# Kernel tuning notes

Hardware: AMD Instinct MI355X
Metric: run time of the kernel (lower is better)

Reference implementation:

```python
import jax, jax.numpy as jnp
import numpy as np

EPS = 1e-6  # LayerNorm eps, added to std as in annotated-transformer LayerNorm


def _layernorm(x, gamma, beta):
    # torch-style: a_2*(x-mean)/(std+eps)+b_2, std is UNBIASED (ddof=1)
    mu = x.mean(axis=-1, keepdims=True)
    std = jnp.sqrt(x.var(axis=-1, ddof=1, keepdims=True))
    return gamma * (x - mu) / (std + EPS) + beta


def setup_inputs() -> dict:
    key = jax.random.key(0)
    ks = jax.random.split(key, 6)
    B, S, E, V = 32, 2048, 512, 32000
    return {
        "hidden_state": jax.random.normal(ks[0], (B, 1, E), jnp.float32),
        "output_sequence": jax.random.randint(ks[1], (B, S), 0, V),
        "emb_out": jax.random.normal(ks[2], (V, E), jnp.float32) * 0.02,
        "W_dec": jax.random.normal(ks[3], (E, E), jnp.float32) / np.sqrt(E),
        "b_dec": jnp.zeros((E,), jnp.float32),
        "gamma": jnp.ones((E,), jnp.float32),
        "beta": jnp.zeros((E,), jnp.float32),
        "W_voc": jax.random.normal(ks[4], (E, V), jnp.float32) / np.sqrt(E),
        "b_voc": jnp.zeros((V,), jnp.float32),
    }


def reference(hidden_state, output_sequence, emb_out, W_dec, b_dec, gamma, beta, W_voc, b_voc):
    E = emb_out.shape[1]
    # Embeddings: lookup scaled by sqrt(embed_dim)
    x = emb_out[output_sequence] * jnp.sqrt(jnp.asarray(E, emb_out.dtype))  # [B,S,E]

    def step(z, xt):  # z: [B,E], xt: [B,E]
        z = z + xt
        z = z + z @ W_dec + b_dec  # decoder_transfer with residual
        z = _layernorm(z, gamma, beta)
        return z, None

    z0 = jnp.zeros((x.shape[0], E), x.dtype)
    z, _ = jax.lax.scan(step, z0, jnp.swapaxes(x, 0, 1))  # scan over S
    z = z[:, None, :]  # [B,1,E]
    # VocabLogits: linear + log_softmax
    y = jax.nn.log_softmax(z @ W_voc + b_voc, axis=-1)  # [B,1,V]
    return z, y
```

## Files before the change

### kernel.cpp

```cpp
#include <hip/hip_runtime.h>
#include <math.h>

typedef float v4 __attribute__((ext_vector_type(4)));
typedef unsigned long long u64;

static constexpr int B_ = 32;
static constexpr int S_ = 2048;
static constexpr int E_ = 512;
static constexpr int V_ = 32000;
static constexpr float EPS_ = 1e-6f;
static constexpr int NH_ = 8;
static constexpr int CH_ = 64;

__global__ __launch_bounds__(1024) void scan2b(
    const int* __restrict__ seq,
    const float* __restrict__ emb,
    const float* __restrict__ Wdec,
    const float* __restrict__ bdec,
    const float* __restrict__ gamma,
    const float* __restrict__ beta,
    float* __restrict__ zout,
    u64* __restrict__ zpub)
{
    __shared__ __align__(16) float zs[E_];
    __shared__ __align__(16) float part[NH_][CH_];
    __shared__ __align__(16) float zmbuf[E_];
    __shared__ int   seq_l[S_];

    const int bid  = blockIdx.x;
    const int b    = bid & 31;
    const int h    = bid >> 5;
    const int c0   = h * CH_;
    const int tid  = threadIdx.x;
    const int wv   = tid >> 6;
    const int lane = tid & 63;
    const int cg   = lane & 15;
    const int sub  = lane >> 4;
    const bool comp = (wv < 8);
    const int row0 = wv * 64 + sub * 16;

    v4 w[16];
    if (comp) {
        const float* wp = Wdec + (size_t)row0 * E_ + c0 + 4 * cg;
        #pragma unroll
        for (int q = 0; q < 16; ++q) {
            const float* p = wp + (size_t)q * E_;
            asm volatile("global_load_dwordx4 %0, %1, off\n\ts_waitcnt vmcnt(0)"
                         : "=v"(w[q]) : "v"(p));
        }
    }

    const int* seqb = seq + (size_t)b * S_;
    for (int i = tid; i < S_; i += 1024) seq_l[i] = seqb[i];

    const float gmm = (tid < E_) ? gamma[tid] : 0.f;
    const float btt = (tid < E_) ? beta[tid] : 0.f;
    const float bdr = (tid < CH_) ? bdec[c0 + tid] : 0.f;
    const float sqrtE = sqrtf(512.0f);
    u64* zpb = zpub + (size_t)b * 2 * E_;

    int fs = 0;
    if (wv >= 8 && wv < 15) { const int j = wv - 8; fs = j + ((j >= h) ? 1 : 0); }

    __syncthreads();
    if (tid < E_) zs[tid] = emb[(size_t)seq_l[0] * E_ + tid] * sqrtE;
    __syncthreads();

    for (int t = 0; t < S_; ++t) {
        const int p = t & 1;
        const unsigned tag = (unsigned)(t + 1);

        float e = 0.f;
        if (comp) {
            const int tn = seq_l[(t + 1 < S_) ? t + 1 : t];
            e = emb[(size_t)tn * E_ + tid];

            const v4 za = *(const v4*)&zs[row0];
            const v4 zb = *(const v4*)&zs[row0 + 4];
            const v4 zc = *(const v4*)&zs[row0 + 8];
            const v4 zd = *(const v4*)&zs[row0 + 12];
            v4 acc = za.x * w[0];
            acc += za.y * w[1];
            acc += za.z * w[2];
            acc += za.w * w[3];
            acc += zb.x * w[4];
            acc += zb.y * w[5];
            acc += zb.z * w[6];
            acc += zb.w * w[7];
            acc += zc.x * w[8];
            acc += zc.y * w[9];
            acc += zc.z * w[10];
            acc += zc.w * w[11];
            acc += zd.x * w[12];
            acc += zd.y * w[13];
            acc += zd.z * w[14];
            acc += zd.w * w[15];
            acc.x += __shfl_down(acc.x, 16);
            acc.y += __shfl_down(acc.y, 16);
            acc.z += __shfl_down(acc.z, 16);
            acc.w += __shfl_down(acc.w, 16);
            acc.x += __shfl_down(acc.x, 32);
            acc.y += __shfl_down(acc.y, 32);
            acc.z += __shfl_down(acc.z, 32);
            acc.w += __shfl_down(acc.w, 32);
            if (lane < 16) *(v4*)&part[wv][4 * cg] = acc;
        }
        __syncthreads();

        if (tid < CH_) {
            const float sum = ((part[0][tid] + part[1][tid])
                             + (part[2][tid] + part[3][tid]))
                            + ((part[4][tid] + part[5][tid])
                             + (part[6][tid] + part[7][tid]));
            const float zmid = zs[c0 + tid] + sum + bdr;
            union { float f; unsigned u; } cv; cv.f = zmid;
            __hip_atomic_store(&zpb[p * E_ + c0 + tid],
                               ((u64)tag << 32) | cv.u,
                               __ATOMIC_RELAXED, __HIP_MEMORY_SCOPE_AGENT);
            zmbuf[c0 + tid] = zmid;
        } else if (wv >= 8 && wv < 15) {
            const u64* ap = &zpb[p * E_ + fs * CH_ + lane];
            u64 s0 = __hip_atomic_load(ap, __ATOMIC_RELAXED,
                                       __HIP_MEMORY_SCOPE_AGENT);
            u64 s1 = __hip_atomic_load(ap, __ATOMIC_RELAXED,
                                       __HIP_MEMORY_SCOPE_AGENT);
            float val = 0.f;
            bool done = false;
            for (;;) {
                if (!done && (unsigned)(s0 >> 32) == tag) {
                    val = __uint_as_float((unsigned)s0); done = true;
                }
                if (__all(done)) break;
                s0 = __hip_atomic_load(ap, __ATOMIC_RELAXED,
                                       __HIP_MEMORY_SCOPE_AGENT);
                if (!done && (unsigned)(s1 >> 32) == tag) {
                    val = __uint_as_float((unsigned)s1); done = true;
                }
                if (__all(done)) break;
                s1 = __hip_atomic_load(ap, __ATOMIC_RELAXED,
                                       __HIP_MEMORY_SCOPE_AGENT);
            }
            zmbuf[fs * CH_ + lane] = val;
        }
        __syncthreads();

        if (comp) {
            float s = 0.f, q2 = 0.f;
            #pragma unroll
            for (int k = 0; k < 8; ++k) {
                const float v = zmbuf[lane + 64 * k];
                s += v; q2 += v * v;
            }
            #pragma unroll
            for (int m = 1; m < 64; m <<= 1) {
                s  += __shfl_xor(s, m);
                q2 += __shfl_xor(q2, m);
            }
            const float mu   = s * (1.0f / E_);
            const float var  = (q2 - s * mu) * (1.0f / (E_ - 1));
            const float invd = 1.0f / (sqrtf(var) + EPS_);
            const float zl   = gmm * (zmbuf[tid] - mu) * invd + btt;
            if (t == S_ - 1) {
                if (h == 0) zout[(size_t)b * E_ + tid] = zl;
            } else {
                zs[tid] = fmaf(e, sqrtE, zl);
            }
        }
    }
}

__global__ __launch_bounds__(512) void logits_k(
    const float* __restrict__ zfin,
    const float* __restrict__ Wvoc,
    const float* __restrict__ bvoc,
    float* __restrict__ y)
{
    const int tid = threadIdx.x;
    const int col = blockIdx.x * 128 + (tid & 127);
    const int bg  = (tid >> 7) * 8;

    float acc[8] = {0.f, 0.f, 0.f, 0.f, 0.f, 0.f, 0.f, 0.f};
    const float* wp = Wvoc + col;
    const float* zp = zfin + (size_t)bg * E_;

    for (int k = 0; k < E_; k += 4) {
        const float w0 = wp[(size_t)(k + 0) * V_];
        const float w1 = wp[(size_t)(k + 1) * V_];
        const float w2 = wp[(size_t)(k + 2) * V_];
        const float w3 = wp[(size_t)(k + 3) * V_];
        #pragma unroll
        for (int g = 0; g < 8; ++g) {
            acc[g] = fmaf(zp[g * E_ + k + 0], w0, acc[g]);
            acc[g] = fmaf(zp[g * E_ + k + 1], w1, acc[g]);
            acc[g] = fmaf(zp[g * E_ + k + 2], w2, acc[g]);
            acc[g] = fmaf(zp[g * E_ + k + 3], w3, acc[g]);
        }
    }
    const float bv = bvoc[col];
    #pragma unroll
    for (int g = 0; g < 8; ++g)
        y[(size_t)(bg + g) * V_ + col] = acc[g] + bv;
}

__global__ __launch_bounds__(1024) void lse_k(
    const float* __restrict__ y, float* __restrict__ corr)
{
    __shared__ float redm[16], redl[16];
    const int b = blockIdx.x;
    const int tid = threadIdx.x;
    const float* row = y + (size_t)b * V_;

    float m = -3.0e38f, l = 0.f;
    for (int v = tid; v < V_; v += 1024) {
        const float x = row[v];
        const float nm = fmaxf(m, x);
        l = l * __expf(m - nm) + __expf(x - nm);
        m = nm;
    }
    #pragma unroll
    for (int off = 32; off > 0; off >>= 1) {
        const float om = __shfl_down(m, off);
        const float ol = __shfl_down(l, off);
        const float nm = fmaxf(m, om);
        l = l * __expf(m - nm) + ol * __expf(om - nm);
        m = nm;
    }
    const int lane = tid & 63, wvv = tid >> 6;
    if (lane == 0) { redm[wvv] = m; redl[wvv] = l; }
    __syncthreads();
    if (tid == 0) {
        float M = redm[0], L = redl[0];
        for (int k = 1; k < 16; ++k) {
            const float nm = fmaxf(M, redm[k]);
            L = L * __expf(M - nm) + redl[k] * __expf(redm[k] - nm);
            M = nm;
        }
        corr[b] = M + logf(L);
    }
}

__global__ __launch_bounds__(256) void fix_k(
    float* __restrict__ y, const float* __restrict__ corr)
{
    const int idx = blockIdx.x * 256 + threadIdx.x;
    const size_t o = (size_t)idx * 4;
    const int b = (int)(o / V_);
    const float cr = corr[b];
    v4 v = *(v4*)(y + o);
    v = v - cr;
    *(v4*)(y + o) = v;
}

extern "C" void kernel_launch(void* const* d_in, const int* in_sizes, int n_in,
                              void* d_out, int out_size, void* d_ws, size_t ws_size,
                              hipStream_t stream)
{
    (void)in_sizes; (void)n_in; (void)out_size; (void)ws_size;
    const int*   seq  = (const int*)  d_in[1];
    const float* emb  = (const float*)d_in[2];
    const float* Wdec = (const float*)d_in[3];
    const float* bdec = (const float*)d_in[4];
    const float* gam  = (const float*)d_in[5];
    const float* bet  = (const float*)d_in[6];
    const float* Wvoc = (const float*)d_in[7];
    const float* bvoc = (const float*)d_in[8];

    float* out  = (float*)d_out;
    float* zout = out;
    float* y    = out + B_ * E_;

    const size_t exch_u64 = (size_t)B_ * 2 * E_;
    u64*   zpub = (u64*)d_ws;
    float* corr = (float*)((char*)d_ws + exch_u64 * sizeof(u64));

    hipMemsetAsync(zpub, 0, exch_u64 * sizeof(u64), stream);

    hipLaunchKernelGGL(scan2b, dim3(B_ * NH_), dim3(1024), 0, stream,
                       seq, emb, Wdec, bdec, gam, bet, zout, zpub);
    hipLaunchKernelGGL(logits_k, dim3(V_ / 128), dim3(512), 0, stream,
                       zout, Wvoc, bvoc, y);
    hipLaunchKernelGGL(lse_k, dim3(B_), dim3(1024), 0, stream, y, corr);
    hipLaunchKernelGGL(fix_k, dim3(1000), dim3(256), 0, stream, y, corr);
}
```

Baseline: 4.138 ms.

## Fold LayerNorm into decoder matvec and replace block barriers with flag-based sync

The scan kernel is restructured so the LayerNorm of the previous step is folded algebraically into the next matvec: W gets the identity added for the residual, the matvec runs on gamma-scaled unnormalized z, and mean and inverse std are applied afterwards as inv*(M - mu*G) plus the separately computed embedding matvec. Per-step __syncthreads are replaced by LDS flag handshakes between waves. Per-slice partial sums and sums of squares are published through global memory, so a dedicated wave can compute the statistics without a full-vector reduction. This aims to shorten the serial critical path of each recurrence step, at the cost of doing two matvecs per step, a more fragile spin-wait protocol, and different floating-point rounding.

```diff
diff --git a/kernel.cpp b/kernel.cpp
--- a/kernel.cpp
+++ b/kernel.cpp
@@ -12,7 +12,30 @@
 static constexpr int NH_ = 8;
 static constexpr int CH_ = 64;
 
-__global__ __launch_bounds__(1024) void scan2b(
+#define WG_ __HIP_MEMORY_SCOPE_WORKGROUP
+#define AG_ __HIP_MEMORY_SCOPE_AGENT
+
+static __device__ __forceinline__ v4 mv16(const v4* w, const float* zp) {
+    const v4 a = *(const v4*)(zp);
+    const v4 b = *(const v4*)(zp + 4);
+    const v4 c = *(const v4*)(zp + 8);
+    const v4 d = *(const v4*)(zp + 12);
+    v4 acc = a.x * w[0];
+    acc += a.y * w[1];  acc += a.z * w[2];  acc += a.w * w[3];
+    acc += b.x * w[4];  acc += b.y * w[5];  acc += b.z * w[6];  acc += b.w * w[7];
+    acc += c.x * w[8];  acc += c.y * w[9];  acc += c.z * w[10]; acc += c.w * w[11];
+    acc += d.x * w[12]; acc += d.y * w[13]; acc += d.z * w[14]; acc += d.w * w[15];
+    return acc;
+}
+static __device__ __forceinline__ v4 red2(v4 acc) {
+    acc.x += __shfl_down(acc.x, 16); acc.y += __shfl_down(acc.y, 16);
+    acc.z += __shfl_down(acc.z, 16); acc.w += __shfl_down(acc.w, 16);
+    acc.x += __shfl_down(acc.x, 32); acc.y += __shfl_down(acc.y, 32);
+    acc.z += __shfl_down(acc.z, 32); acc.w += __shfl_down(acc.w, 32);
+    return acc;
+}
+
+__global__ __launch_bounds__(1024) void scanfx(
     const int* __restrict__ seq,
     const float* __restrict__ emb,
     const float* __restrict__ Wdec,
@@ -22,10 +45,17 @@
     float* __restrict__ zout,
     u64* __restrict__ zpub)
 {
-    __shared__ __align__(16) float zs[E_];
+    __shared__ __align__(16) float zmG[2][E_];
+    __shared__ __align__(16) float xbuf[2][E_];
     __shared__ __align__(16) float part[NH_][CH_];
-    __shared__ __align__(16) float zmbuf[E_];
-    __shared__ int   seq_l[S_];
+    __shared__ __align__(16) float xpart[NH_][CH_];
+    __shared__ float munv[2][2];
+    __shared__ unsigned vrdy[2][NH_];
+    __shared__ unsigned rdone[NH_];
+    __shared__ unsigned mtag[2];
+    __shared__ unsigned hseen;
+    __shared__ unsigned cnt;
+    __shared__ int seq_l[S_];
 
     const int bid  = blockIdx.x;
     const int b    = bid & 31;
@@ -48,82 +78,127 @@
             asm volatile("global_load_dwordx4 %0, %1, off\n\ts_waitcnt vmcnt(0)"
                          : "=v"(w[q]) : "v"(p));
         }
+        const int cb = c0 + 4 * cg;
+        #pragma unroll
+        for (int q = 0; q < 16; ++q) {
+            const int r = row0 + q;
+            w[q].x += (r == cb + 0) ? 1.f : 0.f;
+            w[q].y += (r == cb + 1) ? 1.f : 0.f;
+            w[q].z += (r == cb + 2) ? 1.f : 0.f;
+            w[q].w += (r == cb + 3) ? 1.f : 0.f;
+        }
     }
 
     const int* seqb = seq + (size_t)b * S_;
     for (int i = tid; i < S_; i += 1024) seq_l[i] = seqb[i];
 
-    const float gmm = (tid < E_) ? gamma[tid] : 0.f;
-    const float btt = (tid < E_) ? beta[tid] : 0.f;
-    const float bdr = (tid < CH_) ? bdec[c0 + tid] : 0.f;
     const float sqrtE = sqrtf(512.0f);
+    const float gmm = comp ? gamma[tid] : 0.f;
+    const float btt = comp ? beta[tid]  : 0.f;
+    const float bd  = (wv == h) ? bdec[c0 + lane]  : 0.f;
+    const float gh  = (wv == h) ? gamma[c0 + lane] : 0.f;
+
+    int fs = 0; float gf = 0.f;
+    if (wv >= 8 && wv < 15) {
+        const int j = wv - 8; fs = j + ((j >= h) ? 1 : 0);
+        gf = gamma[fs * CH_ + lane];
+    }
+
     u64* zpb = zpub + (size_t)b * 2 * E_;
-
-    int fs = 0;
-    if (wv >= 8 && wv < 15) { const int j = wv - 8; fs = j + ((j >= h) ? 1 : 0); }
-
+    u64* zst = zpub + (size_t)B_ * 2 * E_ + (size_t)b * 32;
+
+    if (comp) { zmG[1][tid] = gamma[tid]; zmG[0][tid] = 0.f; }
+    if (tid < NH_) { vrdy[0][tid] = 0u; vrdy[1][tid] = 0u; rdone[tid] = 0u; }
+    if (tid == 0) {
+        mtag[0] = 0u; mtag[1] = 0u;
+        munv[1][0] = 0.f; munv[1][1] = 0.f;
+        munv[0][0] = 0.f; munv[0][1] = 0.f;
+        hseen = 0u; cnt = 0u;
+    }
     __syncthreads();
-    if (tid < E_) zs[tid] = emb[(size_t)seq_l[0] * E_ + tid] * sqrtE;
+    if (comp) xbuf[0][tid] = emb[(size_t)seq_l[0] * E_ + tid] * sqrtE;
+
+    float Gc = 0.f;
+    if (comp) {
+        v4 g = red2(mv16(w, &zmG[1][row0]));
+        if (lane < 16) *(v4*)&part[wv][4 * cg] = g;
+    }
     __syncthreads();
+    if (wv == h) {
+        Gc = ((part[0][lane] + part[1][lane]) + (part[2][lane] + part[3][lane]))
+           + ((part[4][lane] + part[5][lane]) + (part[6][lane] + part[7][lane]));
+    }
+    __syncthreads();
 
     for (int t = 0; t < S_; ++t) {
-        const int p = t & 1;
+        const int pt = t & 1, pp = pt ^ 1;
         const unsigned tag = (unsigned)(t + 1);
 
-        float e = 0.f;
         if (comp) {
-            const int tn = seq_l[(t + 1 < S_) ? t + 1 : t];
-            e = emb[(size_t)tn * E_ + tid];
-
-            const v4 za = *(const v4*)&zs[row0];
-            const v4 zb = *(const v4*)&zs[row0 + 4];
-            const v4 zc = *(const v4*)&zs[row0 + 8];
-            const v4 zd = *(const v4*)&zs[row0 + 12];
-            v4 acc = za.x * w[0];
-            acc += za.y * w[1];
-            acc += za.z * w[2];
-            acc += za.w * w[3];
-            acc += zb.x * w[4];
-            acc += zb.y * w[5];
-            acc += zb.z * w[6];
-            acc += zb.w * w[7];
-            acc += zc.x * w[8];
-            acc += zc.y * w[9];
-            acc += zc.z * w[10];
-            acc += zc.w * w[11];
-            acc += zd.x * w[12];
-            acc += zd.y * w[13];
-            acc += zd.z * w[14];
-            acc += zd.w * w[15];
-            acc.x += __shfl_down(acc.x, 16);
-            acc.y += __shfl_down(acc.y, 16);
-            acc.z += __shfl_down(acc.z, 16);
-            acc.w += __shfl_down(acc.w, 16);
-            acc.x += __shfl_down(acc.x, 32);
-            acc.y += __shfl_down(acc.y, 32);
-            acc.z += __shfl_down(acc.z, 32);
-            acc.w += __shfl_down(acc.w, 32);
-            if (lane < 16) *(v4*)&part[wv][4 * cg] = acc;
-        }
-        __syncthreads();
-
-        if (tid < CH_) {
-            const float sum = ((part[0][tid] + part[1][tid])
-                             + (part[2][tid] + part[3][tid]))
-                            + ((part[4][tid] + part[5][tid])
-                             + (part[6][tid] + part[7][tid]));
-            const float zmid = zs[c0 + tid] + sum + bdr;
-            union { float f; unsigned u; } cv; cv.f = zmid;
-            __hip_atomic_store(&zpb[p * E_ + c0 + tid],
-                               ((u64)tag << 32) | cv.u,
-                               __ATOMIC_RELAXED, __HIP_MEMORY_SCOPE_AGENT);
-            zmbuf[c0 + tid] = zmid;
-        } else if (wv >= 8 && wv < 15) {
-            const u64* ap = &zpb[p * E_ + fs * CH_ + lane];
-            u64 s0 = __hip_atomic_load(ap, __ATOMIC_RELAXED,
-                                       __HIP_MEMORY_SCOPE_AGENT);
-            u64 s1 = __hip_atomic_load(ap, __ATOMIC_RELAXED,
-                                       __HIP_MEMORY_SCOPE_AGENT);
+            const int tok = seq_l[(t + 1 < S_) ? t + 1 : t];
+            const float ev = emb[(size_t)tok * E_ + tid];
+
+            v4 xacc = mv16(w, &xbuf[pt][row0]);
+
+            while (__hip_atomic_load(&vrdy[pp][wv], __ATOMIC_ACQUIRE, WG_)
+                   != (unsigned)t) __builtin_amdgcn_s_sleep(1);
+            v4 macc = mv16(w, &zmG[pp][row0]);
+            if (lane == 0)
+                __hip_atomic_store(&rdone[wv], tag, __ATOMIC_RELEASE, WG_);
+
+            macc = red2(macc); xacc = red2(xacc);
+            if (lane < 16) {
+                *(v4*)&part[wv][4 * cg]  = macc;
+                *(v4*)&xpart[wv][4 * cg] = xacc;
+            }
+            if (lane == 0)
+                __hip_atomic_fetch_add(&cnt, 1u, __ATOMIC_RELEASE, WG_);
+
+            xbuf[pt ^ 1][tid] = fmaf(ev, sqrtE, btt);
+
+            if (wv == h) {
+                while (__hip_atomic_load(&cnt, __ATOMIC_ACQUIRE, WG_)
+                       < 8u * tag) {}
+                const float Mr =
+                    ((part[0][lane] + part[1][lane]) + (part[2][lane] + part[3][lane]))
+                  + ((part[4][lane] + part[5][lane]) + (part[6][lane] + part[7][lane]));
+                const float Xr =
+                    ((xpart[0][lane] + xpart[1][lane]) + (xpart[2][lane] + xpart[3][lane]))
+                  + ((xpart[4][lane] + xpart[5][lane]) + (xpart[6][lane] + xpart[7][lane]));
+                while (__hip_atomic_load(&mtag[pp], __ATOMIC_ACQUIRE, WG_)
+                       != (unsigned)t) __builtin_amdgcn_s_sleep(1);
+                const float mu  = munv[pp][0];
+                const float inv = munv[pp][1];
+                __hip_atomic_store(&hseen, tag, __ATOMIC_RELEASE, WG_);
+
+                const float zmid = inv * (Mr - mu * Gc) + Xr + bd;
+                union { float f; unsigned u; } cv; cv.f = zmid;
+                __hip_atomic_store(&zpb[pt * E_ + c0 + lane],
+                                   ((u64)tag << 32) | cv.u,
+                                   __ATOMIC_RELAXED, AG_);
+                zmG[pt][c0 + lane] = zmid * gh;
+                asm volatile("s_waitcnt lgkmcnt(0)" ::: "memory");
+                if (lane == 0)
+                    __hip_atomic_store(&vrdy[pt][h], tag, __ATOMIC_RELEASE, WG_);
+
+                float s = zmid, q2 = zmid * zmid;
+                #pragma unroll
+                for (int m = 1; m < 64; m <<= 1) {
+                    s  += __shfl_xor(s, m);
+                    q2 += __shfl_xor(q2, m);
+                }
+                if (lane == 0) {
+                    union { float f; unsigned u; } c1, c2; c1.f = s; c2.f = q2;
+                    __hip_atomic_store(&zst[pt * 16 + 0 + h],
+                                       ((u64)tag << 32) | c1.u, __ATOMIC_RELAXED, AG_);
+                    __hip_atomic_store(&zst[pt * 16 + 8 + h],
+                                       ((u64)tag << 32) | c2.u, __ATOMIC_RELAXED, AG_);
+                }
+            }
+        } else if (wv < 15) {
+            const u64* ap = &zpb[pt * E_ + fs * CH_ + lane];
+            u64 s0 = __hip_atomic_load(ap, __ATOMIC_RELAXED, AG_);
+            u64 s1 = __hip_atomic_load(ap, __ATOMIC_RELAXED, AG_);
             float val = 0.f;
             bool done = false;
             for (;;) {
@@ -131,41 +206,59 @@
                     val = __uint_as_float((unsigned)s0); done = true;
                 }
                 if (__all(done)) break;
-                s0 = __hip_atomic_load(ap, __ATOMIC_RELAXED,
-                                       __HIP_MEMORY_SCOPE_AGENT);
+                s0 = __hip_atomic_load(ap, __ATOMIC_RELAXED, AG_);
                 if (!done && (unsigned)(s1 >> 32) == tag) {
                     val = __uint_as_float((unsigned)s1); done = true;
                 }
                 if (__all(done)) break;
-                s1 = __hip_atomic_load(ap, __ATOMIC_RELAXED,
-                                       __HIP_MEMORY_SCOPE_AGENT);
+                s1 = __hip_atomic_load(ap, __ATOMIC_RELAXED, AG_);
             }
-            zmbuf[fs * CH_ + lane] = val;
-        }
-        __syncthreads();
-
-        if (comp) {
-            float s = 0.f, q2 = 0.f;
-            #pragma unroll
-            for (int k = 0; k < 8; ++k) {
-                const float v = zmbuf[lane + 64 * k];
-                s += v; q2 += v * v;
+            while (__hip_atomic_load(&rdone[fs], __ATOMIC_ACQUIRE, WG_)
+                   < (unsigned)t) __builtin_amdgcn_s_sleep(1);
+            zmG[pt][fs * CH_ + lane] = val * gf;
+            asm volatile("s_waitcnt lgkmcnt(0)" ::: "memory");
+            if (lane == 0)
+                __hip_atomic_store(&vrdy[pt][fs], tag, __ATOMIC_RELEASE, WG_);
+        } else {
+            const bool need = (lane < 16);
+            const u64* ap = &zst[pt * 16 + lane];
+            bool done = !need; float sv = 0.f;
+            do {
+                if (!done) {
+                    const u64 v = __hip_atomic_load(ap, __ATOMIC_RELAXED, AG_);
+                    if ((unsigned)(v >> 32) == tag) {
+                        sv = __uint_as_float((unsigned)v); done = true;
+                    }
+                }
+            } while (!__all(done));
+            sv += __shfl_xor(sv, 1);
+            sv += __shfl_xor(sv, 2);
+            sv += __shfl_xor(sv, 4);
+            const float St = sv;
+            const float Qt = __shfl(sv, 8);
+            const float mu  = St * (1.0f / E_);
+            const float var = (Qt - St * mu) * (1.0f / (E_ - 1));
+            const float inv = 1.0f / (sqrtf(var) + EPS_);
+            while (__hip_atomic_load(&hseen, __ATOMIC_ACQUIRE, WG_)
+                   < (unsigned)t) __builtin_amdgcn_s_sleep(1);
+            if (lane == 0) {
+                munv[pt][0] = mu; munv[pt][1] = inv;
+                asm volatile("s_waitcnt lgkmcnt(0)" ::: "memory");
+                __hip_atomic_store(&mtag[pt], tag, __ATOMIC_RELEASE, WG_);
             }
-            #pragma unroll
-            for (int m = 1; m < 64; m <<= 1) {
-                s  += __shfl_xor(s, m);
-                q2 += __shfl_xor(q2, m);
-            }
-            const float mu   = s * (1.0f / E_);
-            const float var  = (q2 - s * mu) * (1.0f / (E_ - 1));
-            const float invd = 1.0f / (sqrtf(var) + EPS_);
-            const float zl   = gmm * (zmbuf[tid] - mu) * invd + btt;
-            if (t == S_ - 1) {
-                if (h == 0) zout[(size_t)b * E_ + tid] = zl;
-            } else {
-                zs[tid] = fmaf(e, sqrtE, zl);
-            }
-        }
+        }
+    }
+
+    if (h == 0 && comp) {
+        const int pf = (S_ - 1) & 1;
+        const unsigned ftag = (unsigned)S_;
+        while (__hip_atomic_load(&vrdy[pf][wv], __ATOMIC_ACQUIRE, WG_)
+               != ftag) __builtin_amdgcn_s_sleep(1);
+        while (__hip_atomic_load(&mtag[pf], __ATOMIC_ACQUIRE, WG_)
+               != ftag) __builtin_amdgcn_s_sleep(1);
+        const float mu  = munv[pf][0];
+        const float inv = munv[pf][1];
+        zout[(size_t)b * E_ + tid] = inv * (zmG[pf][tid] - mu * gmm) + btt;
     }
 }
 
@@ -269,13 +362,13 @@
     float* zout = out;
     float* y    = out + B_ * E_;
 
-    const size_t exch_u64 = (size_t)B_ * 2 * E_;
+    const size_t exch_u64 = (size_t)B_ * 2 * E_ + (size_t)B_ * 32;
     u64*   zpub = (u64*)d_ws;
     float* corr = (float*)((char*)d_ws + exch_u64 * sizeof(u64));
 
     hipMemsetAsync(zpub, 0, exch_u64 * sizeof(u64), stream);
 
-    hipLaunchKernelGGL(scan2b, dim3(B_ * NH_), dim3(1024), 0, stream,
+    hipLaunchKernelGGL(scanfx, dim3(B_ * NH_), dim3(1024), 0, stream,
                        seq, emb, Wdec, bdec, gam, bet, zout, zpub);
     hipLaunchKernelGGL(logits_k, dim3(V_ / 128), dim3(512), 0, stream,
                        zout, Wvoc, bvoc, y);
```

New measurement: 7.398 ms. +78.8%, slower.
